# Kernel optimization log

Hardware: AMD Instinct MI355X
Metric: run time of the kernel (lower is better)

## Reference

```python
import jax, jax.numpy as jnp
import numpy as np


def setup_inputs() -> dict:
    key = jax.random.key(0)
    ks = jax.random.split(key, 9)
    B, D, E, H, C = 8192, 1024, 8, 4096, 10
    s = lambda fan_in: 1.0 / np.sqrt(fan_in)
    return {
        "x":  jax.random.normal(ks[0], (B, D), jnp.float32),
        "Wr": jax.random.normal(ks[1], (D, E), jnp.float32) * s(D),
        "br": jnp.zeros((E,), jnp.float32),
        "W1": jax.random.normal(ks[2], (E, D, H), jnp.float32) * s(D),
        "b1": jnp.zeros((E, H), jnp.float32),
        "W2": jax.random.normal(ks[3], (E, H, D), jnp.float32) * s(H),
        "b2": jnp.zeros((E, D), jnp.float32),
        "Wc": jax.random.normal(ks[4], (D, C), jnp.float32) * s(D),
        "bc": jnp.zeros((C,), jnp.float32),
    }


def reference(x, Wr, br, W1, b1, W2, b2, Wc, bc):
    # Dense (no-topology) MoE path: softmax routing over all experts.
    routing = jax.nn.softmax(x @ Wr + br, axis=-1)          # [B, E]
    # All experts run on every token (dense all-expert loop, vectorized).
    h = jax.nn.relu(jnp.einsum('bd,edh->ebh', x, W1) + b1[:, None, :])  # [E, B, H]
    y = jnp.einsum('ebh,ehd->ebd', h, W2) + b2[:, None, :]              # [E, B, D]
    # Routing-weighted accumulation: sum_e y[e] * routing[:, e]
    out = jnp.einsum('ebd,be->bd', y, routing)              # [B, D]
    return out @ Wc + bc                                    # [B, C]
```

## Files before the change

### kernel.cpp

```cpp
#include <hip/hip_runtime.h>
#include <cstdint>
#include <cstddef>

using bf16x8 = __attribute__((ext_vector_type(8))) short;
using f32x4  = __attribute__((ext_vector_type(4))) float;

constexpr int kB = 8192;
constexpr int kD = 1024;
constexpr int kE = 8;
constexpr int kH = 4096;
constexpr int kC = 10;

__device__ __forceinline__ unsigned short f2bf(float f) {
  unsigned int u = __float_as_uint(f);
  u += 0x7FFFu + ((u >> 16) & 1u);
  return (unsigned short)(u >> 16);
}

#define GLD16(gptr, lptr)                                                      \
  __builtin_amdgcn_global_load_lds(                                            \
      (const __attribute__((address_space(1))) void*)(gptr),                   \
      (__attribute__((address_space(3))) void*)(lptr), 16, 0, 0)

#define SBAR()                                                                 \
  do {                                                                         \
    asm volatile("s_waitcnt lgkmcnt(0)" ::: "memory");                         \
    __builtin_amdgcn_s_barrier();                                              \
    asm volatile("" ::: "memory");                                             \
    __builtin_amdgcn_sched_barrier(0);                                         \
  } while (0)

__device__ __forceinline__ int lbyte(int row, int j) {
  const int s = row >> 1;
  const int jp = (((row & 1) << 2) | j) ^ (s & 7);
  return s * 128 + jp * 16;
}

__global__ __launch_bounds__(256) void k_convert_x(const float* __restrict__ x,
                                                   unsigned short* __restrict__ xb) {
  const long i = ((long)blockIdx.x * 256 + threadIdx.x) * 8;
  float4 a = *reinterpret_cast<const float4*>(x + i);
  float4 b = *reinterpret_cast<const float4*>(x + i + 4);
  bf16x8 o;
  o[0] = (short)f2bf(a.x); o[1] = (short)f2bf(a.y);
  o[2] = (short)f2bf(a.z); o[3] = (short)f2bf(a.w);
  o[4] = (short)f2bf(b.x); o[5] = (short)f2bf(b.y);
  o[6] = (short)f2bf(b.z); o[7] = (short)f2bf(b.w);
  *reinterpret_cast<bf16x8*>(xb + i) = o;
}

__global__ __launch_bounds__(256) void k_transpose_w(const float* __restrict__ W,
                                                     unsigned short* __restrict__ Wt,
                                                     int K, int N) {
  __shared__ unsigned short tile[32][33];
  const int e = blockIdx.z;
  const int n0 = blockIdx.x * 32, k0 = blockIdx.y * 32;
  const int tx = threadIdx.x, ty = threadIdx.y;
  const float* Wb = W + (size_t)e * K * N;
  unsigned short* Wtb = Wt + (size_t)e * N * K;
#pragma unroll
  for (int j = 0; j < 32; j += 8)
    tile[ty + j][tx] = f2bf(Wb[(size_t)(k0 + ty + j) * N + n0 + tx]);
  __syncthreads();
#pragma unroll
  for (int j = 0; j < 32; j += 8)
    Wtb[(size_t)(n0 + ty + j) * K + k0 + tx] = tile[tx][ty + j];
}

__global__ __launch_bounds__(256) void k_routing(const float* __restrict__ x,
                                                 const float* __restrict__ Wr,
                                                 const float* __restrict__ br,
                                                 float* __restrict__ r) {
  const int w = threadIdx.x >> 6, l = threadIdx.x & 63;
  const int b = blockIdx.x * 4 + w;
  const float* xr = x + (size_t)b * kD;
  float acc[kE];
#pragma unroll
  for (int e = 0; e < kE; ++e) acc[e] = 0.f;
  for (int d = l; d < kD; d += 64) {
    const float xv = xr[d];
    const float* wrow = Wr + d * kE;
#pragma unroll
    for (int e = 0; e < kE; ++e) acc[e] += xv * wrow[e];
  }
#pragma unroll
  for (int e = 0; e < kE; ++e) {
#pragma unroll
    for (int s = 32; s > 0; s >>= 1) acc[e] += __shfl_xor(acc[e], s);
    acc[e] += br[e];
  }
  float mx = acc[0];
#pragma unroll
  for (int e = 1; e < kE; ++e) mx = fmaxf(mx, acc[e]);
  float sum = 0.f;
#pragma unroll
  for (int e = 0; e < kE; ++e) { acc[e] = expf(acc[e] - mx); sum += acc[e]; }
  const float inv = 1.f / sum;
  float val = 0.f;
#pragma unroll
  for (int e = 0; e < kE; ++e) if (l == e) val = acc[e] * inv;
  if (l < kE) r[(size_t)b * kE + l] = val;
}

__global__ __launch_bounds__(128) void k_vbuild(const float* __restrict__ W2,
                                                const float* __restrict__ Wc,
                                                unsigned short* __restrict__ Vt) {
  __shared__ float WcL[kD * kC];
  for (int i = threadIdx.x; i < kD * kC; i += 128) WcL[i] = Wc[i];
  __syncthreads();
  const int gid = blockIdx.x * 128 + threadIdx.x;
  const int e = gid >> 12, hrow = gid & 4095;
  const float4* w2row = reinterpret_cast<const float4*>(W2 + (size_t)gid * kD);
  float acc[kC];
#pragma unroll
  for (int c = 0; c < kC; ++c) acc[c] = 0.f;
  for (int i = 0; i < kD / 4; ++i) {
    float4 w = w2row[i];
    const float* wc0 = WcL + (i * 4) * kC;
#pragma unroll
    for (int c = 0; c < kC; ++c)
      acc[c] += w.x * wc0[c] + w.y * wc0[kC + c] + w.z * wc0[2 * kC + c] +
                w.w * wc0[3 * kC + c];
  }
  unsigned short* vte = Vt + (size_t)e * 16 * kH;
#pragma unroll
  for (int c = 0; c < kC; ++c) vte[(size_t)c * kH + hrow] = f2bf(acc[c]);
#pragma unroll
  for (int c = kC; c < 16; ++c) vte[(size_t)c * kH + hrow] = 0;
}

__global__ __launch_bounds__(128) void k_ubuild(const float* __restrict__ b2,
                                                const float* __restrict__ Wc,
                                                float* __restrict__ u) {
  const int t = threadIdx.x;
  if (t >= kE * kC) return;
  const int e = t / kC, c = t % kC;
  float acc = 0.f;
  for (int d = 0; d < kD; ++d) acc += b2[e * kD + d] * Wc[d * kC + c];
  u[e * 16 + c] = acc;
}

__global__ __launch_bounds__(256) void k_zero_f32(float* __restrict__ p) {
  p[(size_t)blockIdx.x * 256 + threadIdx.x] = 0.f;
}

__global__ __launch_bounds__(256, 3) void k_moe_fused(
    const unsigned short* __restrict__ xb,
    const unsigned short* __restrict__ W1t,
    const float* __restrict__ b1,
    const unsigned short* __restrict__ Vt,
    const float* __restrict__ rr,
    float* __restrict__ part) {
  __shared__ __align__(16) char smem[49152];
  constexpr int K = kD, BK = 32, NT = K / BK;

  const int e = blockIdx.z;
  const int bx = (blockIdx.x & 7) * 8 + (blockIdx.x >> 3);
  const int brow = bx * 128, bcol = blockIdx.y * 128;
  const unsigned short* const A = xb;
  const unsigned short* const Bt = W1t + (size_t)e * kH * kD;

  const int tid = threadIdx.x;
  const int l = tid & 63, w = tid >> 6;
  const int wr = w >> 1, wc = w & 1;
  const int fr = l & 15, jg = l >> 4;

  const int jsup = (tid & 7) ^ ((tid >> 3) & 7);
  const int row0 = (((tid >> 3) << 1) | (jsup >> 2));
  const int sj = jsup & 3;
  const size_t gA0 = (size_t)(brow + row0) * K + sj * 8;
  const size_t gA1 = (size_t)(brow + 64 + row0) * K + sj * 8;
  const size_t gB0 = (size_t)(bcol + row0) * K + sj * 8;
  const size_t gB1 = (size_t)(bcol + 64 + row0) * K + sj * 8;
  const int wb0 = w * 1024, wb1 = 4096 + w * 1024;

#define STAGE(bufbyte, kt)                                                     \
  do {                                                                         \
    GLD16(A + gA0 + (size_t)(kt) * BK, smem + (bufbyte) + wb0);                \
    GLD16(A + gA1 + (size_t)(kt) * BK, smem + (bufbyte) + wb1);                \
    GLD16(Bt + gB0 + (size_t)(kt) * BK, smem + (bufbyte) + 8192 + wb0);        \
    GLD16(Bt + gB1 + (size_t)(kt) * BK, smem + (bufbyte) + 8192 + wb1);        \
  } while (0)

  int offA[4], offB[4];
#pragma unroll
  for (int m = 0; m < 4; ++m) offA[m] = lbyte(wr * 64 + m * 16 + fr, jg);
#pragma unroll
  for (int n = 0; n < 4; ++n) offB[n] = lbyte(wc * 64 + n * 16 + fr, jg);

  f32x4 acc[4][4];
#pragma unroll
  for (int m = 0; m < 4; ++m)
#pragma unroll
    for (int n = 0; n < 4; ++n) acc[m][n] = (f32x4){0.f, 0.f, 0.f, 0.f};

  STAGE(0, 0);
  STAGE(16384, 1);
  asm volatile("s_waitcnt vmcnt(4)" ::: "memory");
  __builtin_amdgcn_s_barrier();
  asm volatile("" ::: "memory");
  __builtin_amdgcn_sched_barrier(0);

  int bufb = 0;
  for (int t = 0; t < NT; ++t) {
    int nxt = bufb + 16384; if (nxt == 49152) nxt = 0;
    int n2 = nxt + 16384;  if (n2 == 49152) n2 = 0;
    if (t + 2 < NT) STAGE(n2, t + 2);

    const char* const Ab = smem + bufb;
    const char* const Bb = smem + bufb + 8192;
    bf16x8 av[4], bv[4];
#pragma unroll
    for (int m = 0; m < 4; ++m) av[m] = *reinterpret_cast<const bf16x8*>(Ab + offA[m]);
#pragma unroll
    for (int n = 0; n < 4; ++n) bv[n] = *reinterpret_cast<const bf16x8*>(Bb + offB[n]);
    __builtin_amdgcn_s_setprio(1);
#pragma unroll
    for (int m = 0; m < 4; ++m)
#pragma unroll
      for (int n = 0; n < 4; ++n)
        acc[m][n] = __builtin_amdgcn_mfma_f32_16x16x32_bf16(av[m], bv[n], acc[m][n], 0, 0, 0);
    __builtin_amdgcn_s_setprio(0);

    if (t < NT - 1) {
      if (t + 2 < NT) asm volatile("s_waitcnt vmcnt(4)" ::: "memory");
      else            asm volatile("s_waitcnt vmcnt(0)" ::: "memory");
      SBAR();
    }
    bufb = nxt;
  }
#undef STAGE

  SBAR();

  float b1v[4];
#pragma unroll
  for (int n = 0; n < 4; ++n)
    b1v[n] = b1[(size_t)e * kH + bcol + wc * 64 + n * 16 + fr];

#pragma unroll
  for (int m = 0; m < 4; ++m) {
#pragma unroll
    for (int n = 0; n < 4; ++n) {
      const int colh = wc * 64 + n * 16 + fr;
#pragma unroll
      for (int j = 0; j < 4; ++j) {
        const int row = wr * 64 + m * 16 + (jg << 2) + j;
        const float v = fmaxf(acc[m][n][j] + b1v[n], 0.f);
        *reinterpret_cast<unsigned short*>(
            smem + row * 256 + ((colh * 2) ^ ((row & 7) << 4))) = f2bf(v);
      }
    }
  }
  SBAR();

  const unsigned short* const VtE = Vt + (size_t)e * 16 * kH;
  bf16x8 gvk[4];
#pragma unroll
  for (int kk = 0; kk < 4; ++kk)
    gvk[kk] = *reinterpret_cast<const bf16x8*>(VtE + (size_t)fr * kH + bcol + kk * 32 + jg * 8);

  f32x4 pc[2];
  pc[0] = (f32x4){0.f, 0.f, 0.f, 0.f};
  pc[1] = (f32x4){0.f, 0.f, 0.f, 0.f};
#pragma unroll
  for (int f = 0; f < 2; ++f) {
    const int rowl = (2 * w + f) * 16 + fr;
#pragma unroll
    for (int kk = 0; kk < 4; ++kk) {
      bf16x8 ga = *reinterpret_cast<const bf16x8*>(
          smem + rowl * 256 + ((kk * 64 + jg * 16) ^ ((rowl & 7) << 4)));
      pc[f] = __builtin_amdgcn_mfma_f32_16x16x32_bf16(ga, gvk[kk], pc[f], 0, 0, 0);
    }
  }

#pragma unroll
  for (int f = 0; f < 2; ++f) {
    const int rowg = brow + (2 * w + f) * 16 + (jg << 2);
#pragma unroll
    for (int j = 0; j < 4; ++j) {
      const float val = pc[f][j] * rr[(size_t)(rowg + j) * kE + e];
      atomicAdd(&part[(size_t)(rowg + j) * 16 + fr], val);
    }
  }
}

__global__ __launch_bounds__(256) void k_combine(const float* __restrict__ part,
                                                 const float* __restrict__ rr,
                                                 const float* __restrict__ u,
                                                 const float* __restrict__ bc,
                                                 float* __restrict__ y) {
  const int tid = threadIdx.x;
  const int rloc = tid >> 4, c = tid & 15;
  const int b = blockIdx.x * 16 + rloc;
  if (c >= kC) return;
  float acc = part[(size_t)b * 16 + c] + bc[c];
#pragma unroll
  for (int e = 0; e < kE; ++e) acc += rr[(size_t)b * kE + e] * u[e * 16 + c];
  y[(size_t)b * kC + c] = acc;
}

extern "C" void kernel_launch(void* const* d_in, const int* in_sizes, int n_in,
                              void* d_out, int out_size, void* d_ws, size_t ws_size,
                              hipStream_t stream) {
  (void)in_sizes; (void)n_in; (void)out_size; (void)ws_size;
  const float* x  = (const float*)d_in[0];
  const float* Wr = (const float*)d_in[1];
  const float* br = (const float*)d_in[2];
  const float* W1 = (const float*)d_in[3];
  const float* b1 = (const float*)d_in[4];
  const float* W2 = (const float*)d_in[5];
  const float* b2 = (const float*)d_in[6];
  const float* Wc = (const float*)d_in[7];
  const float* bc = (const float*)d_in[8];
  float* y = (float*)d_out;

  char* p = (char*)d_ws;
  unsigned short* xb  = (unsigned short*)p; p += (size_t)kB * kD * 2;
  unsigned short* W1t = (unsigned short*)p; p += (size_t)kE * kH * kD * 2;
  unsigned short* Vt  = (unsigned short*)p; p += (size_t)kE * 16 * kH * 2;
  float* r    = (float*)p;                  p += (size_t)kB * kE * 4;
  float* u    = (float*)p;                  p += (size_t)kE * 16 * 4;
  float* part = (float*)p;                  p += (size_t)kB * 16 * 4;

  k_convert_x<<<dim3(kB * kD / 8 / 256), dim3(256), 0, stream>>>(x, xb);
  k_routing<<<dim3(kB / 4), dim3(256), 0, stream>>>(x, Wr, br, r);
  k_transpose_w<<<dim3(kH / 32, kD / 32, kE), dim3(32, 8), 0, stream>>>(W1, W1t, kD, kH);
  k_vbuild<<<dim3(kE * kH / 128), dim3(128), 0, stream>>>(W2, Wc, Vt);
  k_ubuild<<<dim3(1), dim3(128), 0, stream>>>(b2, Wc, u);
  k_zero_f32<<<dim3(kB * 16 / 256), dim3(256), 0, stream>>>(part);

  k_moe_fused<<<dim3(kB / 128, kH / 128, kE), dim3(256), 0, stream>>>(
      xb, W1t, b1, Vt, r, part);

  k_combine<<<dim3(kB / 16), dim3(256), 0, stream>>>(part, r, u, bc, y);
}
```

Baseline: 759.7 us.

## Enlarge fused MoE GEMM tile to 256x256 with 8 waves and interleaved staging

The fused expert GEMM moves from 128x128 tiles with 4 waves and a triple-buffered BK=32 pipeline to 256x256 tiles with 8 waves and 128KB of double-buffered LDS holding BK=64 slices. Global-to-LDS staging for A and B is spread across four MFMA sub-phases per buffer, separated by explicit barriers, so memory traffic overlaps compute. Each output tile now reuses operands over twice as many rows and columns, which cuts global and L2 traffic per FLOP. The cost is a single resident block per CU because of LDS use, higher register pressure from 32 accumulator fragments, and more barriers per k-step.

```diff
diff --git a/kernel.cpp b/kernel.cpp
--- a/kernel.cpp
+++ b/kernel.cpp
@@ -21,20 +21,6 @@
   __builtin_amdgcn_global_load_lds(                                            \
       (const __attribute__((address_space(1))) void*)(gptr),                   \
       (__attribute__((address_space(3))) void*)(lptr), 16, 0, 0)
-
-#define SBAR()                                                                 \
-  do {                                                                         \
-    asm volatile("s_waitcnt lgkmcnt(0)" ::: "memory");                         \
-    __builtin_amdgcn_s_barrier();                                              \
-    asm volatile("" ::: "memory");                                             \
-    __builtin_amdgcn_sched_barrier(0);                                         \
-  } while (0)
-
-__device__ __forceinline__ int lbyte(int row, int j) {
-  const int s = row >> 1;
-  const int jp = (((row & 1) << 2) | j) ^ (s & 7);
-  return s * 128 + jp * 16;
-}
 
 __global__ __launch_bounds__(256) void k_convert_x(const float* __restrict__ x,
                                                    unsigned short* __restrict__ xb) {
@@ -144,142 +130,170 @@
   p[(size_t)blockIdx.x * 256 + threadIdx.x] = 0.f;
 }
 
-__global__ __launch_bounds__(256, 3) void k_moe_fused(
+__global__ __launch_bounds__(512, 2) void k_moe_fused256(
     const unsigned short* __restrict__ xb,
     const unsigned short* __restrict__ W1t,
     const float* __restrict__ b1,
     const unsigned short* __restrict__ Vt,
     const float* __restrict__ rr,
     float* __restrict__ part) {
-  __shared__ __align__(16) char smem[49152];
-  constexpr int K = kD, BK = 32, NT = K / BK;
+  __shared__ __align__(16) char smem[131072];
+  constexpr int K = kD;
+  constexpr int NIT = K / 128;
 
   const int e = blockIdx.z;
-  const int bx = (blockIdx.x & 7) * 8 + (blockIdx.x >> 3);
-  const int brow = bx * 128, bcol = blockIdx.y * 128;
-  const unsigned short* const A = xb;
+  const int bx = (blockIdx.x & 7) * 4 + (blockIdx.x >> 3);
+  const int brow = bx * 256, bcol = blockIdx.y * 256;
+  const unsigned short* const At = xb;
   const unsigned short* const Bt = W1t + (size_t)e * kH * kD;
 
   const int tid = threadIdx.x;
-  const int l = tid & 63, w = tid >> 6;
-  const int wr = w >> 1, wc = w & 1;
+  const int w = tid >> 6, l = tid & 63;
+  const int wr = w >> 2, wc = w & 3;
   const int fr = l & 15, jg = l >> 4;
 
-  const int jsup = (tid & 7) ^ ((tid >> 3) & 7);
-  const int row0 = (((tid >> 3) << 1) | (jsup >> 2));
-  const int sj = jsup & 3;
-  const size_t gA0 = (size_t)(brow + row0) * K + sj * 8;
-  const size_t gA1 = (size_t)(brow + 64 + row0) * K + sj * 8;
-  const size_t gB0 = (size_t)(bcol + row0) * K + sj * 8;
-  const size_t gB1 = (size_t)(bcol + 64 + row0) * K + sj * 8;
-  const int wb0 = w * 1024, wb1 = 4096 + w * 1024;
-
-#define STAGE(bufbyte, kt)                                                     \
-  do {                                                                         \
-    GLD16(A + gA0 + (size_t)(kt) * BK, smem + (bufbyte) + wb0);                \
-    GLD16(A + gA1 + (size_t)(kt) * BK, smem + (bufbyte) + wb1);                \
-    GLD16(Bt + gB0 + (size_t)(kt) * BK, smem + (bufbyte) + 8192 + wb0);        \
-    GLD16(Bt + gB1 + (size_t)(kt) * BK, smem + (bufbyte) + 8192 + wb1);        \
-  } while (0)
-
-  int offA[4], offB[4];
-#pragma unroll
-  for (int m = 0; m < 4; ++m) offA[m] = lbyte(wr * 64 + m * 16 + fr, jg);
-#pragma unroll
-  for (int n = 0; n < 4; ++n) offB[n] = lbyte(wc * 64 + n * 16 + fr, jg);
-
-  f32x4 acc[4][4];
-#pragma unroll
-  for (int m = 0; m < 4; ++m)
+  int ck[2];
+#pragma unroll
+  for (int k = 0; k < 2; ++k) ck[k] = (((k * 4 + jg) ^ (fr & 7)) << 4);
+  const int abase = wr * 16384;
+  const int bbase = 32768 + (wc >> 1) * 16384;
+  const int brow0 = (wc & 1) * 64;
+
+  const int p0 = w * 64 + l;
+  const int rp = p0 >> 3;
+  const int cs = (p0 & 7) ^ (rp & 7);
+  const size_t aofs = (size_t)(brow + rp) * K + cs * 8;
+  const size_t bofs = (size_t)(bcol + rp) * K + cs * 8;
+  const int ldst = w * 1024;
+
+#define STG_A(buf, ht, kt)                                                     \
+  do {                                                                         \
+    GLD16(At + aofs + (size_t)(ht) * 131072 + (size_t)(kt) * 64,               \
+          smem + (buf) * 65536 + (ht) * 16384 + ldst);                         \
+    GLD16(At + aofs + (size_t)(ht) * 131072 + 65536 + (size_t)(kt) * 64,       \
+          smem + (buf) * 65536 + (ht) * 16384 + 8192 + ldst);                  \
+  } while (0)
+#define STG_B(buf, ht, kt)                                                     \
+  do {                                                                         \
+    GLD16(Bt + bofs + (size_t)(ht) * 131072 + (size_t)(kt) * 64,               \
+          smem + (buf) * 65536 + 32768 + (ht) * 16384 + ldst);                 \
+    GLD16(Bt + bofs + (size_t)(ht) * 131072 + 65536 + (size_t)(kt) * 64,       \
+          smem + (buf) * 65536 + 32768 + (ht) * 16384 + 8192 + ldst);          \
+  } while (0)
+
+#define READ_A(buf, mp)                                                        \
+  do {                                                                         \
+    _Pragma("unroll") for (int mm = 0; mm < 2; ++mm)                           \
+    _Pragma("unroll") for (int k = 0; k < 2; ++k)                              \
+      aq[mm][k] = *reinterpret_cast<const bf16x8*>(                            \
+          smem + (buf) * 65536 + abase + (((mp) * 2 + mm) * 16 + fr) * 128 + ck[k]); \
+  } while (0)
+#define READ_B(buf)                                                            \
+  do {                                                                         \
+    _Pragma("unroll") for (int n = 0; n < 4; ++n)                              \
+    _Pragma("unroll") for (int k = 0; k < 2; ++k)                              \
+      bq[n][k] = *reinterpret_cast<const bf16x8*>(                             \
+          smem + (buf) * 65536 + bbase + (brow0 + n * 16 + fr) * 128 + ck[k]); \
+  } while (0)
+#define MFMA16(mp)                                                             \
+  do {                                                                         \
+    __builtin_amdgcn_s_setprio(1);                                             \
+    _Pragma("unroll") for (int mm = 0; mm < 2; ++mm)                           \
+    _Pragma("unroll") for (int n = 0; n < 4; ++n)                              \
+    _Pragma("unroll") for (int k = 0; k < 2; ++k)                              \
+      acc[(mp) * 2 + mm][n] = __builtin_amdgcn_mfma_f32_16x16x32_bf16(         \
+          aq[mm][k], bq[n][k], acc[(mp) * 2 + mm][n], 0, 0, 0);                \
+    __builtin_amdgcn_s_setprio(0);                                             \
+  } while (0)
+#define BARW() asm volatile("s_barrier\ns_waitcnt lgkmcnt(0)" ::: "memory")
+#define BARP() asm volatile("s_barrier" ::: "memory")
+
+  bf16x8 aq[2][2], bq[4][2];
+  f32x4 acc[8][4];
+#pragma unroll
+  for (int m = 0; m < 8; ++m)
 #pragma unroll
     for (int n = 0; n < 4; ++n) acc[m][n] = (f32x4){0.f, 0.f, 0.f, 0.f};
 
-  STAGE(0, 0);
-  STAGE(16384, 1);
+  STG_A(0, 0, 0); STG_A(0, 1, 0); STG_B(0, 0, 0); STG_B(0, 1, 0);
+  STG_B(1, 0, 1); STG_B(1, 1, 1);
   asm volatile("s_waitcnt vmcnt(4)" ::: "memory");
-  __builtin_amdgcn_s_barrier();
-  asm volatile("" ::: "memory");
-  __builtin_amdgcn_sched_barrier(0);
-
-  int bufb = 0;
-  for (int t = 0; t < NT; ++t) {
-    int nxt = bufb + 16384; if (nxt == 49152) nxt = 0;
-    int n2 = nxt + 16384;  if (n2 == 49152) n2 = 0;
-    if (t + 2 < NT) STAGE(n2, t + 2);
-
-    const char* const Ab = smem + bufb;
-    const char* const Bb = smem + bufb + 8192;
-    bf16x8 av[4], bv[4];
-#pragma unroll
-    for (int m = 0; m < 4; ++m) av[m] = *reinterpret_cast<const bf16x8*>(Ab + offA[m]);
-#pragma unroll
-    for (int n = 0; n < 4; ++n) bv[n] = *reinterpret_cast<const bf16x8*>(Bb + offB[n]);
-    __builtin_amdgcn_s_setprio(1);
-#pragma unroll
-    for (int m = 0; m < 4; ++m)
-#pragma unroll
-      for (int n = 0; n < 4; ++n)
-        acc[m][n] = __builtin_amdgcn_mfma_f32_16x16x32_bf16(av[m], bv[n], acc[m][n], 0, 0, 0);
-    __builtin_amdgcn_s_setprio(0);
-
-    if (t < NT - 1) {
-      if (t + 2 < NT) asm volatile("s_waitcnt vmcnt(4)" ::: "memory");
-      else            asm volatile("s_waitcnt vmcnt(0)" ::: "memory");
-      SBAR();
-    }
-    bufb = nxt;
-  }
-#undef STAGE
-
-  SBAR();
-
-  float b1v[4];
-#pragma unroll
-  for (int n = 0; n < 4; ++n)
-    b1v[n] = b1[(size_t)e * kH + bcol + wc * 64 + n * 16 + fr];
-
-#pragma unroll
-  for (int m = 0; m < 4; ++m) {
-#pragma unroll
-    for (int n = 0; n < 4; ++n) {
-      const int colh = wc * 64 + n * 16 + fr;
+  BARP();
+
+  for (int i = 0; i < NIT; ++i) {
+    const bool g = (i < NIT - 1);
+    const int kx = 2 * i + 2, ky = 2 * i + 3;
+    READ_A(0, 0); READ_B(0);
+    STG_A(1, 0, 2 * i + 1);
+    BARW(); MFMA16(0); BARP();
+    READ_A(0, 1);
+    STG_A(1, 1, 2 * i + 1);
+    if (g) STG_B(0, 0, kx);
+    BARW(); MFMA16(1); BARP();
+    READ_A(0, 2);
+    if (g) STG_B(0, 1, kx);
+    BARW(); MFMA16(2); BARP();
+    READ_A(0, 3);
+    BARW(); MFMA16(3);
+    if (g) asm volatile("s_waitcnt vmcnt(4)" ::: "memory");
+    else   asm volatile("s_waitcnt vmcnt(0)" ::: "memory");
+    BARP();
+    READ_A(1, 0); READ_B(1);
+    if (g) { STG_A(0, 0, kx); STG_A(0, 1, kx); }
+    BARW(); MFMA16(0); BARP();
+    READ_A(1, 1);
+    if (g) STG_B(1, 0, ky);
+    BARW(); MFMA16(1); BARP();
+    READ_A(1, 2);
+    if (g) STG_B(1, 1, ky);
+    BARW(); MFMA16(2); BARP();
+    READ_A(1, 3);
+    BARW(); MFMA16(3);
+    if (g) asm volatile("s_waitcnt vmcnt(4)" ::: "memory");
+    BARP();
+  }
+#undef STG_A
+#undef STG_B
+#undef READ_A
+#undef READ_B
+
+#pragma unroll
+  for (int n = 0; n < 4; ++n) {
+    const int lcol = wc * 64 + n * 16 + fr;
+    const float bias = b1[(size_t)e * kH + bcol + lcol];
+    const int cbyte = (lcol >> 3) << 4;
+#pragma unroll
+    for (int m = 0; m < 8; ++m) {
 #pragma unroll
       for (int j = 0; j < 4; ++j) {
-        const int row = wr * 64 + m * 16 + (jg << 2) + j;
-        const float v = fmaxf(acc[m][n][j] + b1v[n], 0.f);
+        const int lrow = wr * 128 + m * 16 + jg * 4 + j;
+        const float v = fmaxf(acc[m][n][j] + bias, 0.f);
         *reinterpret_cast<unsigned short*>(
-            smem + row * 256 + ((colh * 2) ^ ((row & 7) << 4))) = f2bf(v);
+            smem + lrow * 512 + (cbyte ^ ((lrow & 7) << 4)) + (fr & 7) * 2) = f2bf(v);
       }
     }
   }
-  SBAR();
-
-  const unsigned short* const VtE = Vt + (size_t)e * 16 * kH;
-  bf16x8 gvk[4];
-#pragma unroll
-  for (int kk = 0; kk < 4; ++kk)
-    gvk[kk] = *reinterpret_cast<const bf16x8*>(VtE + (size_t)fr * kH + bcol + kk * 32 + jg * 8);
-
-  f32x4 pc[2];
-  pc[0] = (f32x4){0.f, 0.f, 0.f, 0.f};
-  pc[1] = (f32x4){0.f, 0.f, 0.f, 0.f};
+  asm volatile("s_waitcnt lgkmcnt(0)\ns_barrier" ::: "memory");
+
+  const unsigned short* const VtE = Vt + (size_t)e * 16 * kH + (size_t)fr * kH + bcol;
+  bf16x8 gv[8];
+#pragma unroll
+  for (int kk = 0; kk < 8; ++kk)
+    gv[kk] = *reinterpret_cast<const bf16x8*>(VtE + kk * 32 + jg * 8);
 #pragma unroll
   for (int f = 0; f < 2; ++f) {
     const int rowl = (2 * w + f) * 16 + fr;
-#pragma unroll
-    for (int kk = 0; kk < 4; ++kk) {
+    f32x4 pc = (f32x4){0.f, 0.f, 0.f, 0.f};
+#pragma unroll
+    for (int kk = 0; kk < 8; ++kk) {
       bf16x8 ga = *reinterpret_cast<const bf16x8*>(
-          smem + rowl * 256 + ((kk * 64 + jg * 16) ^ ((rowl & 7) << 4)));
-      pc[f] = __builtin_amdgcn_mfma_f32_16x16x32_bf16(ga, gvk[kk], pc[f], 0, 0, 0);
+          smem + rowl * 512 + ((((kk * 4 + jg)) ^ (rowl & 7)) << 4));
+      pc = __builtin_amdgcn_mfma_f32_16x16x32_bf16(ga, gv[kk], pc, 0, 0, 0);
     }
-  }
-
-#pragma unroll
-  for (int f = 0; f < 2; ++f) {
-    const int rowg = brow + (2 * w + f) * 16 + (jg << 2);
+    const int rowg = brow + (2 * w + f) * 16 + jg * 4;
 #pragma unroll
     for (int j = 0; j < 4; ++j) {
-      const float val = pc[f][j] * rr[(size_t)(rowg + j) * kE + e];
+      const float val = pc[j] * rr[(size_t)(rowg + j) * kE + e];
       atomicAdd(&part[(size_t)(rowg + j) * 16 + fr], val);
     }
   }
@@ -330,7 +344,7 @@
   k_ubuild<<<dim3(1), dim3(128), 0, stream>>>(b2, Wc, u);
   k_zero_f32<<<dim3(kB * 16 / 256), dim3(256), 0, stream>>>(part);
 
-  k_moe_fused<<<dim3(kB / 128, kH / 128, kE), dim3(256), 0, stream>>>(
+  k_moe_fused256<<<dim3(kB / 256, kH / 256, kE), dim3(512), 0, stream>>>(
       xb, W1t, b1, Vt, r, part);
 
   k_combine<<<dim3(kB / 16), dim3(256), 0, stream>>>(part, r, u, bc, y);
```

After: 697.8 us. 8.1% less time.
